# Kernel optimization log

Measured on AMD Instinct MI355X. Metric: run time of the kernel, lower is better.

The kernel has to match this reference:

```python
import jax, jax.numpy as jnp
import numpy as np

N_HEADS = 16
LN_EPS = 1e-6


def _mha(q_in, kv_in, mask, wq, bq, wk, bk, wv, bv, wo, bo):
    B, Sq, D = q_in.shape
    H = N_HEADS
    dh = D // H
    def split(x):  # [B,S,D] -> [B,H,S,dh]
        return x.reshape(B, -1, H, dh).transpose(0, 2, 1, 3)
    q = split(q_in @ wq + bq)
    k = split(kv_in @ wk + bk)
    v = split(kv_in @ wv + bv)
    scores = jnp.einsum('bhqd,bhkd->bhqk', q, k) / jnp.sqrt(jnp.asarray(dh, q.dtype))
    scores = scores + mask * (-1e9)
    attn = jax.nn.softmax(scores, axis=-1)
    out = jnp.einsum('bhqk,bhkd->bhqd', attn, v)
    out = out.transpose(0, 2, 1, 3).reshape(B, Sq, D)
    return out @ wo + bo


def _layer_norm(x, gamma, beta):
    mu = jnp.mean(x, axis=-1, keepdims=True)
    var = jnp.mean(jnp.square(x - mu), axis=-1, keepdims=True)
    return (x - mu) * jax.lax.rsqrt(var + LN_EPS) * gamma + beta


def setup_inputs() -> dict:
    key = jax.random.key(0)
    B, S_dec, S_enc, D, F = 4, 1024, 1024, 1024, 4096
    ks = jax.random.split(key, 16)
    s = 0.02
    inp = {
        'inputs': jax.random.normal(ks[0], (B, S_dec, D), jnp.float32),
        'enc_outputs': jax.random.normal(ks[1], (B, S_enc, D), jnp.float32),
        # causal look-ahead mask: 1 above diagonal -> -1e9 added to scores
        'mask_1': jnp.triu(jnp.ones((S_dec, S_dec), jnp.float32), k=1)[None, None],
        'mask_2': jnp.zeros((B, 1, 1, S_enc), jnp.float32),
    }
    names = ['wq1', 'wk1', 'wv1', 'wo1', 'wq2', 'wk2', 'wv2', 'wo2']
    for i, n in enumerate(names):
        inp[n] = jax.random.normal(ks[2 + i], (D, D), jnp.float32) * s
        inp['b' + n[1:]] = jnp.zeros((D,), jnp.float32)
    inp['w_ff1'] = jax.random.normal(ks[10], (D, F), jnp.float32) * s
    inp['b_ff1'] = jnp.zeros((F,), jnp.float32)
    inp['w_ff2'] = jax.random.normal(ks[11], (F, D), jnp.float32) * s
    inp['b_ff2'] = jnp.zeros((D,), jnp.float32)
    for i in (1, 2, 3):
        inp[f'g{i}'] = jnp.ones((D,), jnp.float32)
        inp[f'beta{i}'] = jnp.zeros((D,), jnp.float32)
    return inp


def reference(inputs, enc_outputs, mask_1, mask_2,
              wq1, bq1, wk1, bk1, wv1, bv1, wo1, bo1,
              wq2, bq2, wk2, bk2, wv2, bv2, wo2, bo2,
              w_ff1, b_ff1, w_ff2, b_ff2,
              g1, beta1, g2, beta2, g3, beta3):
    # causal self-attention + residual + LN (dropout inactive at inference)
    attn = _mha(inputs, inputs, mask_1, wq1, bq1, wk1, bk1, wv1, bv1, wo1, bo1)
    attn = _layer_norm(attn + inputs, g1, beta1)
    # encoder-decoder cross-attention + residual + LN
    attn2 = _mha(attn, enc_outputs, mask_2, wq2, bq2, wk2, bk2, wv2, bv2, wo2, bo2)
    attn2 = _layer_norm(attn2 + attn, g2, beta2)
    # FFN + residual + LN
    h = jax.nn.relu(attn2 @ w_ff1 + b_ff1)
    h = h @ w_ff2 + b_ff2
    return _layer_norm(h + attn2, g3, beta3)
```

## Files before the change

kernel.cpp:

```cpp
#include <hip/hip_runtime.h>
#include <stdint.h>

typedef unsigned short ushort_t;
typedef __attribute__((ext_vector_type(8))) short bf16x8;
typedef __attribute__((ext_vector_type(4))) float f32x4;
typedef __attribute__((ext_vector_type(4))) unsigned short us4;

#define DEV __device__ __forceinline__

DEV unsigned short f2bf(float f) {
  union { float f; unsigned u; } x; x.f = f;
  unsigned r = x.u + 0x7fffu + ((x.u >> 16) & 1u);
  return (unsigned short)(r >> 16);
}

DEV void gload16(const void* g, void* l) {
  __builtin_amdgcn_global_load_lds(
      (const __attribute__((address_space(1))) unsigned int*)g,
      (__attribute__((address_space(3))) unsigned int*)l, 16, 0, 0);
}

#define MFMA16 __builtin_amdgcn_mfma_f32_16x16x32_bf16

__global__ __launch_bounds__(256) void cast_bf16_kernel(
    const float* __restrict__ x, ushort_t* __restrict__ y, int n4) {
  int i = blockIdx.x * 256 + threadIdx.x;
  if (i >= n4) return;
  float4 v = ((const float4*)x)[i];
  us4 o; o.x = f2bf(v.x); o.y = f2bf(v.y); o.z = f2bf(v.z); o.w = f2bf(v.w);
  ((us4*)y)[i] = o;
}

__global__ __launch_bounds__(256) void reduce_cast_kernel(
    const float* __restrict__ p0, const float* __restrict__ p1,
    ushort_t* __restrict__ y, int n4) {
  int i = blockIdx.x * 256 + threadIdx.x;
  if (i >= n4) return;
  float4 a = ((const float4*)p0)[i];
  float4 b = ((const float4*)p1)[i];
  us4 o; o.x = f2bf(a.x + b.x); o.y = f2bf(a.y + b.y);
  o.z = f2bf(a.z + b.z); o.w = f2bf(a.w + b.w);
  ((us4*)y)[i] = o;
}

__global__ __launch_bounds__(256) void transpose_cast_kernel(
    const float* __restrict__ W, ushort_t* __restrict__ dst, int K, int N) {
  __shared__ float tile[64][65];
  int n0 = blockIdx.x * 64, k0 = blockIdx.y * 64;
  int tid = threadIdx.x;
#pragma unroll
  for (int it = 0; it < 16; ++it) {
    int idx = it * 256 + tid; int r = idx >> 6, c = idx & 63;
    tile[r][c] = W[(size_t)(k0 + r) * N + n0 + c];
  }
  __syncthreads();
#pragma unroll
  for (int it = 0; it < 16; ++it) {
    int idx = it * 256 + tid; int r = idx >> 6, c = idx & 63;
    dst[(size_t)(n0 + r) * K + k0 + c] = f2bf(tile[c][r]);
  }
}

struct Src8 { const float* p[8]; };
__global__ __launch_bounds__(256) void transpose_cast8_kernel(
    Src8 s, ushort_t* __restrict__ dst) {
  __shared__ float tile[64][65];
  const float* W = s.p[blockIdx.z];
  ushort_t* out = dst + (size_t)blockIdx.z * 1048576;
  int n0 = blockIdx.x * 64, k0 = blockIdx.y * 64;
  int tid = threadIdx.x;
#pragma unroll
  for (int it = 0; it < 16; ++it) {
    int idx = it * 256 + tid; int r = idx >> 6, c = idx & 63;
    tile[r][c] = W[(size_t)(k0 + r) * 1024 + n0 + c];
  }
  __syncthreads();
#pragma unroll
  for (int it = 0; it < 16; ++it) {
    int idx = it * 256 + tid; int r = idx >> 6, c = idx & 63;
    out[(size_t)(n0 + r) * 1024 + k0 + c] = f2bf(tile[c][r]);
  }
}

__global__ __launch_bounds__(256) void transpose_v_kernel(
    const ushort_t* __restrict__ V, int ldv, ushort_t* __restrict__ vT) {
  __shared__ ushort_t tile[64][65];
  int s0 = blockIdx.x * 64;
  int bh = blockIdx.y;
  int b = bh >> 4, h = bh & 15;
  int tid = threadIdx.x;
#pragma unroll
  for (int it = 0; it < 4; ++it) {
    int idx = it * 256 + tid; int r = idx >> 4, c = (idx & 15) * 4;
    us4 v = *(const us4*)&V[(size_t)(b * 1024 + s0 + r) * ldv + h * 64 + c];
    tile[r][c] = v.x; tile[r][c + 1] = v.y; tile[r][c + 2] = v.z; tile[r][c + 3] = v.w;
  }
  __syncthreads();
#pragma unroll
  for (int it = 0; it < 4; ++it) {
    int idx = it * 256 + tid; int r = idx >> 4, c = (idx & 15) * 4;
    us4 o; o.x = tile[c][r]; o.y = tile[c + 1][r]; o.z = tile[c + 2][r]; o.w = tile[c + 3][r];
    *(us4*)&vT[((size_t)bh * 64 + r) * 1024 + s0 + c] = o;
  }
}

template <int WF32, int WB16, int RELU>
__global__ __launch_bounds__(256, 2) void gemm_bt(
    const ushort_t* __restrict__ A, const ushort_t* __restrict__ Bt,
    const float* __restrict__ b0, const float* __restrict__ b1,
    const float* __restrict__ b2, const float* __restrict__ b3,
    float* __restrict__ Cf, ushort_t* __restrict__ Cb,
    int M, int N, int K, int Ks, long long pstr) {
  __shared__ ushort_t sA[4096];
  __shared__ ushort_t sB[4096];
  const int tid = threadIdx.x;
  const int w = tid >> 6, lane = tid & 63;
  const int lrow = lane & 15, lk = lane >> 4;
  const int m0 = blockIdx.x * 128, n0 = blockIdx.y * 128;
  const int kz = blockIdx.z * Ks;
  const int wr = w >> 1, wc = w & 1;
  f32x4 acc[4][4] = {};
  const int brow0 = (w * 1024 + lane * 16) >> 6;
  const int kbyte = (lane * 16) & 63;

  for (int kt = kz; kt < kz + Ks; kt += 32) {
    __syncthreads();
    const ushort_t* ga = A + (size_t)(m0 + brow0) * K + kt + (kbyte >> 1);
    gload16(ga, (char*)sA + w * 1024);
    gload16(ga + (size_t)64 * K, (char*)sA + 4096 + w * 1024);
    const ushort_t* gb = Bt + (size_t)(n0 + brow0) * K + kt + (kbyte >> 1);
    gload16(gb, (char*)sB + w * 1024);
    gload16(gb + (size_t)64 * K, (char*)sB + 4096 + w * 1024);
    __syncthreads();
    bf16x8 aF[4], bF[4];
#pragma unroll
    for (int t = 0; t < 4; ++t) {
      aF[t] = *(const bf16x8*)((const char*)sA + ((wr * 64 + t * 16 + lrow) << 6) + (lk << 4));
      bF[t] = *(const bf16x8*)((const char*)sB + ((wc * 64 + t * 16 + lrow) << 6) + (lk << 4));
    }
#pragma unroll
    for (int mt = 0; mt < 4; ++mt)
#pragma unroll
      for (int nt = 0; nt < 4; ++nt)
        acc[mt][nt] = MFMA16(aF[mt], bF[nt], acc[mt][nt], 0, 0, 0);
  }
  float* Cfz = Cf + (long long)blockIdx.z * pstr;
#pragma unroll
  for (int nt = 0; nt < 4; ++nt) {
    int col = n0 + wc * 64 + nt * 16 + lrow;
    int seg = col >> 10;
    const float* bp = seg == 0 ? b0 : seg == 1 ? b1 : seg == 2 ? b2 : b3;
    float bv = bp[col & 1023];
    if (blockIdx.z != 0) bv = 0.f;
#pragma unroll
    for (int mt = 0; mt < 4; ++mt) {
      int rowb = m0 + wr * 64 + mt * 16 + lk * 4;
#pragma unroll
      for (int j = 0; j < 4; ++j) {
        float v = acc[mt][nt][j] + bv;
        if (RELU) v = fmaxf(v, 0.f);
        size_t idx = (size_t)(rowb + j) * N + col;
        if (WF32) Cfz[idx] = v;
        if (WB16) Cb[idx] = f2bf(v);
      }
    }
  }
}

template <int WF32, int WB16, int RELU>
__global__ __launch_bounds__(512, 1) void gemm256(
    const ushort_t* __restrict__ A, const ushort_t* __restrict__ Bt,
    const float* __restrict__ b0, const float* __restrict__ b1,
    const float* __restrict__ b2, const float* __restrict__ b3,
    float* __restrict__ Cf, ushort_t* __restrict__ Cb,
    int M, int N, int K, int Ks, long long pstr) {
  extern __shared__ char L[];
  const int tid = threadIdx.x;
  const int w = tid >> 6, lane = tid & 63;
  const int lrow = lane & 15, lk = lane >> 4;
  const int wm = w >> 2, wn = w & 3;
  const int m0 = blockIdx.x * 256, n0 = blockIdx.y * 256;
  const int kz = blockIdx.z * Ks;
  const int nt = Ks >> 6;

  const int srow = w * 8 + (lane >> 3);
  const int gsw = (lane & 7) ^ ((lane >> 3) & 7);
  const ushort_t* srcA = A + (size_t)(m0 + srow) * K + kz + gsw * 8;
  const ushort_t* srcB = Bt + (size_t)(n0 + srow) * K + kz + gsw * 8;
  const int dstw = w * 1024;

#define STG(M_, T_)                                                   \
  do {                                                                \
    const ushort_t* g0 = ((M_) ? srcB : srcA) + (size_t)(T_) * 64;    \
    char* d_ = L + (((T_) & 1) << 16) + ((M_) << 15) + dstw;          \
    gload16(g0, d_);                                                  \
    gload16(g0 + (size_t)64 * K, d_ + 8192);                          \
    gload16(g0 + (size_t)128 * K, d_ + 16384);                        \
    gload16(g0 + (size_t)192 * K, d_ + 24576);                        \
  } while (0)

  f32x4 acc[8][4] = {};
  const int swz = (lrow & 7) << 4;
  const int k0b = (lk << 4) ^ swz;
  const int k1b = (64 + (lk << 4)) ^ swz;
  const int aBase = (wm * 128 + lrow) << 7;
  const int bBase = ((wn * 64 + lrow) << 7) + 32768;

  STG(0, 0); STG(1, 0); STG(0, 1);
  asm volatile("s_waitcnt vmcnt(4)" ::: "memory");
  __builtin_amdgcn_s_barrier();

  for (int t = 0; t < nt; ++t) {
    const int buf = (t & 1) << 16;
    const char* base = L + buf;
    bf16x8 aF[8], bF0, bF1;
    {
#pragma unroll
      for (int m = 0; m < 8; ++m) aF[m] = *(const bf16x8*)(base + aBase + m * 2048 + k0b);
      bF0 = *(const bf16x8*)(base + bBase + k0b);
      bF1 = *(const bf16x8*)(base + bBase + 2048 + k0b);
      if (t + 1 < nt) STG(1, t + 1);
      __builtin_amdgcn_s_barrier();
      __builtin_amdgcn_s_setprio(1);
#pragma unroll
      for (int m = 0; m < 8; ++m) {
        acc[m][0] = MFMA16(aF[m], bF0, acc[m][0], 0, 0, 0);
        acc[m][1] = MFMA16(aF[m], bF1, acc[m][1], 0, 0, 0);
      }
      __builtin_amdgcn_s_setprio(0);
      __builtin_amdgcn_s_barrier();
    }
    {
      bF0 = *(const bf16x8*)(base + bBase + 4096 + k0b);
      bF1 = *(const bf16x8*)(base + bBase + 6144 + k0b);
      __builtin_amdgcn_s_barrier();
      __builtin_amdgcn_s_setprio(1);
#pragma unroll
      for (int m = 0; m < 8; ++m) {
        acc[m][2] = MFMA16(aF[m], bF0, acc[m][2], 0, 0, 0);
        acc[m][3] = MFMA16(aF[m], bF1, acc[m][3], 0, 0, 0);
      }
      __builtin_amdgcn_s_setprio(0);
      __builtin_amdgcn_s_barrier();
    }
    {
#pragma unroll
      for (int m = 0; m < 8; ++m) aF[m] = *(const bf16x8*)(base + aBase + m * 2048 + k1b);
      bF0 = *(const bf16x8*)(base + bBase + k1b);
      bF1 = *(const bf16x8*)(base + bBase + 2048 + k1b);
      __builtin_amdgcn_s_barrier();
      __builtin_amdgcn_s_setprio(1);
#pragma unroll
      for (int m = 0; m < 8; ++m) {
        acc[m][0] = MFMA16(aF[m], bF0, acc[m][0], 0, 0, 0);
        acc[m][1] = MFMA16(aF[m], bF1, acc[m][1], 0, 0, 0);
      }
      __builtin_amdgcn_s_setprio(0);
      __builtin_amdgcn_s_barrier();
    }
    {
      bF0 = *(const bf16x8*)(base + bBase + 4096 + k1b);
      bF1 = *(const bf16x8*)(base + bBase + 6144 + k1b);
      if (t + 2 < nt) {
        STG(0, t + 2);
        asm volatile("s_waitcnt vmcnt(4)" ::: "memory");
      } else {
        asm volatile("s_waitcnt vmcnt(0)" ::: "memory");
      }
      __builtin_amdgcn_s_barrier();
      __builtin_amdgcn_s_setprio(1);
#pragma unroll
      for (int m = 0; m < 8; ++m) {
        acc[m][2] = MFMA16(aF[m], bF0, acc[m][2], 0, 0, 0);
        acc[m][3] = MFMA16(aF[m], bF1, acc[m][3], 0, 0, 0);
      }
      __builtin_amdgcn_s_setprio(0);
      __builtin_amdgcn_s_barrier();
    }
  }
#undef STG

  float* Cfz = Cf + (long long)blockIdx.z * pstr;
#pragma unroll
  for (int n = 0; n < 4; ++n) {
    int col = n0 + wn * 64 + n * 16 + lrow;
    int seg = col >> 10;
    const float* bp = seg == 0 ? b0 : seg == 1 ? b1 : seg == 2 ? b2 : b3;
    float bv = bp[col & 1023];
    if (blockIdx.z != 0) bv = 0.f;
#pragma unroll
    for (int m = 0; m < 8; ++m) {
      int rowb = m0 + wm * 128 + m * 16 + lk * 4;
#pragma unroll
      for (int j = 0; j < 4; ++j) {
        float v = acc[m][n][j] + bv;
        if (RELU) v = fmaxf(v, 0.f);
        size_t idx = (size_t)(rowb + j) * N + col;
        if (WF32) Cfz[idx] = v;
        if (WB16) Cb[idx] = f2bf(v);
      }
    }
  }
}

template <int CAUSAL>
__global__ __launch_bounds__(256, 4) void attn_kernel(
    const ushort_t* __restrict__ Q, int ldq,
    const ushort_t* __restrict__ Kp, int ldk,
    const ushort_t* __restrict__ vT,
    const float* __restrict__ mask2,
    ushort_t* __restrict__ O) {
  __shared__ ushort_t sK[2][4096];
  __shared__ ushort_t sV[2][4096];
  __shared__ ushort_t sP[4][1024];
  const int bh = blockIdx.x, qb = blockIdx.y;
  const int b = bh >> 4, h = bh & 15;
  const int tid = threadIdx.x, w = tid >> 6, lane = tid & 63;
  const int lrow = lane & 15, lk = lane >> 4;

  const ushort_t* qptr = Q + (size_t)(b * 1024 + qb * 64 + w * 16 + lrow) * ldq + h * 64 + lk * 8;
  bf16x8 qF0 = *(const bf16x8*)qptr;
  bf16x8 qF1 = *(const bf16x8*)(qptr + 32);
  f32x4 oacc[4] = {};
  float m_ = -3.0e38f, l_ = 0.f;
  const int nkb = CAUSAL ? (qb + 1) : 16;
  const float C = 0.18033688011112042f;

  const int sr = w * 16 + (lane >> 3);
  const int scb = (((lane & 7) ^ (lane >> 3)) * 16);
  const ushort_t* kbase = Kp + (size_t)(b * 1024 + sr) * ldk + h * 64 + (scb >> 1);
  const ushort_t* vbase = vT + ((size_t)bh * 64 + sr) * 1024 + (scb >> 1);
  char* dstK0 = (char*)sK[0] + w * 2048;
  char* dstV0 = (char*)sV[0] + w * 2048;

#define STAGE(kb_, bufi)                                              \
  do {                                                                \
    const ushort_t* gk = kbase + (size_t)(kb_) * 64 * ldk;            \
    gload16(gk, dstK0 + (bufi) * 8192);                               \
    gload16(gk + (size_t)8 * ldk, dstK0 + (bufi) * 8192 + 1024);      \
    const ushort_t* gv = vbase + (kb_) * 64;                          \
    gload16(gv, dstV0 + (bufi) * 8192);                               \
    gload16(gv + (size_t)8 * 1024, dstV0 + (bufi) * 8192 + 1024);     \
  } while (0)

  STAGE(0, 0);
  const int swz = (lrow & 7) << 4;

  for (int kb = 0; kb < nkb; ++kb) {
    const int buf = kb & 1;
    __syncthreads();
    if (kb + 1 < nkb) STAGE(kb + 1, buf ^ 1);

    const char* kB = (const char*)sK[buf];
    const char* vB = (const char*)sV[buf];
    f32x4 sc[4];
    __builtin_amdgcn_s_setprio(1);
#pragma unroll
    for (int kt = 0; kt < 4; ++kt) {
      const char* rp = kB + ((kt * 16 + lrow) << 7);
      bf16x8 k0 = *(const bf16x8*)(rp + ((lk * 16) ^ swz));
      bf16x8 k1 = *(const bf16x8*)(rp + ((64 + lk * 16) ^ swz));
      f32x4 z = {};
      z = MFMA16(k0, qF0, z, 0, 0, 0);
      sc[kt] = MFMA16(k1, qF1, z, 0, 0, 0);
    }
    __builtin_amdgcn_s_setprio(0);
    if (CAUSAL) {
      if (kb == qb) {
        int ql = w * 16 + lrow;
#pragma unroll
        for (int kt = 0; kt < 4; ++kt)
#pragma unroll
          for (int j = 0; j < 4; ++j)
            if (kt * 16 + lk * 4 + j > ql) sc[kt][j] = -3.0e38f;
      }
    } else {
#pragma unroll
      for (int kt = 0; kt < 4; ++kt) {
        float4 mv = *(const float4*)&mask2[b * 1024 + kb * 64 + kt * 16 + lk * 4];
        sc[kt][0] = fmaf(mv.x, -8e9f, sc[kt][0]);
        sc[kt][1] = fmaf(mv.y, -8e9f, sc[kt][1]);
        sc[kt][2] = fmaf(mv.z, -8e9f, sc[kt][2]);
        sc[kt][3] = fmaf(mv.w, -8e9f, sc[kt][3]);
      }
    }
    float pmax = fmaxf(fmaxf(fmaxf(sc[0][0], sc[0][1]), fmaxf(sc[0][2], sc[0][3])),
                       fmaxf(fmaxf(sc[1][0], sc[1][1]), fmaxf(sc[1][2], sc[1][3])));
    pmax = fmaxf(pmax, fmaxf(fmaxf(fmaxf(sc[2][0], sc[2][1]), fmaxf(sc[2][2], sc[2][3])),
                             fmaxf(fmaxf(sc[3][0], sc[3][1]), fmaxf(sc[3][2], sc[3][3]))));
    pmax = fmaxf(pmax, __shfl_xor(pmax, 16));
    pmax = fmaxf(pmax, __shfl_xor(pmax, 32));
    if (__any(pmax - m_ > 64.f)) {
      float mnew = fmaxf(m_, pmax);
      float scale = __builtin_exp2f((m_ - mnew) * C);
      l_ *= scale;
      m_ = mnew;
#pragma unroll
      for (int j = 0; j < 4; ++j) {
        float sj = __shfl(scale, lk * 4 + j);
        oacc[0][j] *= sj; oacc[1][j] *= sj; oacc[2][j] *= sj; oacc[3][j] *= sj;
      }
    }
    const float mC = m_ * C;
    float ps = 0.f;
#pragma unroll
    for (int kt = 0; kt < 4; ++kt)
#pragma unroll
      for (int j = 0; j < 4; ++j) {
        float e = __builtin_exp2f(fmaf(sc[kt][j], C, -mC));
        sc[kt][j] = e;
        ps += e;
      }
    ps += __shfl_xor(ps, 16);
    ps += __shfl_xor(ps, 32);
    l_ += ps;
    char* bp = (char*)sP[w] + lrow * 128;
#pragma unroll
    for (int kt = 0; kt < 4; ++kt) {
      unsigned d0, d1;
      asm("v_cvt_pk_bf16_f32 %0, %1, %2" : "=v"(d0) : "v"(sc[kt][0]), "v"(sc[kt][1]));
      asm("v_cvt_pk_bf16_f32 %0, %1, %2" : "=v"(d1) : "v"(sc[kt][2]), "v"(sc[kt][3]));
      uint2 dd; dd.x = d0; dd.y = d1;
      *(uint2*)(bp + ((kt * 32 + lk * 8) ^ swz)) = dd;
    }
    bf16x8 pF0 = *(const bf16x8*)(bp + ((lk * 16) ^ swz));
    bf16x8 pF1 = *(const bf16x8*)(bp + ((64 + lk * 16) ^ swz));
    __builtin_amdgcn_s_setprio(1);
#pragma unroll
    for (int t = 0; t < 4; ++t) {
      const char* rp = vB + ((t * 16 + lrow) << 7);
      bf16x8 v0 = *(const bf16x8*)(rp + ((lk * 16) ^ swz));
      bf16x8 v1 = *(const bf16x8*)(rp + ((64 + lk * 16) ^ swz));
      oacc[t] = MFMA16(pF0, v0, oacc[t], 0, 0, 0);
      oacc[t] = MFMA16(pF1, v1, oacc[t], 0, 0, 0);
    }
    __builtin_amdgcn_s_setprio(0);
  }
#undef STAGE
#pragma unroll
  for (int j = 0; j < 4; ++j) {
    float lj = __shfl(l_, lk * 4 + j);
    float invl = 1.f / lj;
    int row = qb * 64 + w * 16 + lk * 4 + j;
    ushort_t* op = O + (size_t)(b * 1024 + row) * 1024 + h * 64;
#pragma unroll
    for (int t = 0; t < 4; ++t) op[t * 16 + lrow] = f2bf(oacc[t][j] * invl);
  }
}

template <int WB16, int NPART>
__global__ __launch_bounds__(256) void ln_kernel(
    const float* __restrict__ p0, const float* __restrict__ p1,
    const float* __restrict__ p2, const float* __restrict__ p3,
    const float* __restrict__ r,
    const float* __restrict__ g, const float* __restrict__ be,
    float* __restrict__ yf, ushort_t* __restrict__ yb) {
  int row = blockIdx.x, tid = threadIdx.x;
  size_t off = (size_t)row * 1024;
  float4 va = ((const float4*)(p0 + off))[tid];
  if (NPART >= 2) {
    float4 t = ((const float4*)(p1 + off))[tid];
    va.x += t.x; va.y += t.y; va.z += t.z; va.w += t.w;
  }
  if (NPART >= 4) {
    float4 t2 = ((const float4*)(p2 + off))[tid];
    float4 t3 = ((const float4*)(p3 + off))[tid];
    va.x += t2.x + t3.x; va.y += t2.y + t3.y;
    va.z += t2.z + t3.z; va.w += t2.w + t3.w;
  }
  float4 vb = ((const float4*)(r + off))[tid];
  float x0 = va.x + vb.x, x1 = va.y + vb.y, x2 = va.z + vb.z, x3 = va.w + vb.w;
  float s = x0 + x1 + x2 + x3;
  float s2 = x0 * x0 + x1 * x1 + x2 * x2 + x3 * x3;
#pragma unroll
  for (int o = 1; o < 64; o <<= 1) { s += __shfl_xor(s, o); s2 += __shfl_xor(s2, o); }
  __shared__ float sh[8];
  if ((tid & 63) == 0) { sh[tid >> 6] = s; sh[4 + (tid >> 6)] = s2; }
  __syncthreads();
  s = sh[0] + sh[1] + sh[2] + sh[3];
  s2 = sh[4] + sh[5] + sh[6] + sh[7];
  float mu = s * 0.0009765625f;
  float var = s2 * 0.0009765625f - mu * mu;
  float inv = rsqrtf(var + 1e-6f);
  float4 gv = ((const float4*)g)[tid];
  float4 bv = ((const float4*)be)[tid];
  float y0 = (x0 - mu) * inv * gv.x + bv.x;
  float y1 = (x1 - mu) * inv * gv.y + bv.y;
  float y2 = (x2 - mu) * inv * gv.z + bv.z;
  float y3 = (x3 - mu) * inv * gv.w + bv.w;
  ((float4*)(yf + off))[tid] = make_float4(y0, y1, y2, y3);
  if (WB16) {
    us4 o; o.x = f2bf(y0); o.y = f2bf(y1); o.z = f2bf(y2); o.w = f2bf(y3);
    ((us4*)(yb + off))[tid] = o;
  }
}

extern "C" void kernel_launch(void* const* d_in, const int* in_sizes, int n_in,
                              void* d_out, int out_size, void* d_ws, size_t ws_size,
                              hipStream_t stream) {
  (void)in_sizes; (void)n_in; (void)out_size; (void)ws_size;
  const float* inputs = (const float*)d_in[0];
  const float* enc    = (const float*)d_in[1];
  const float* mask2  = (const float*)d_in[3];
  const float* wq1 = (const float*)d_in[4];  const float* bq1 = (const float*)d_in[5];
  const float* wk1 = (const float*)d_in[6];  const float* bk1 = (const float*)d_in[7];
  const float* wv1 = (const float*)d_in[8];  const float* bv1 = (const float*)d_in[9];
  const float* wo1 = (const float*)d_in[10]; const float* bo1 = (const float*)d_in[11];
  const float* wq2 = (const float*)d_in[12]; const float* bq2 = (const float*)d_in[13];
  const float* wk2 = (const float*)d_in[14]; const float* bk2 = (const float*)d_in[15];
  const float* wv2 = (const float*)d_in[16]; const float* bv2 = (const float*)d_in[17];
  const float* wo2 = (const float*)d_in[18]; const float* bo2 = (const float*)d_in[19];
  const float* wff1 = (const float*)d_in[20]; const float* bff1 = (const float*)d_in[21];
  const float* wff2 = (const float*)d_in[22]; const float* bff2 = (const float*)d_in[23];
  const float* g1 = (const float*)d_in[24]; const float* be1 = (const float*)d_in[25];
  const float* g2 = (const float*)d_in[26]; const float* be2 = (const float*)d_in[27];
  const float* g3 = (const float*)d_in[28]; const float* be3 = (const float*)d_in[29];

  char* ws = (char*)d_ws;
  const size_t MB = 1024 * 1024;
  const size_t W1M = 1048576;
  ushort_t* wt    = (ushort_t*)ws;
  ushort_t* xb    = (ushort_t*)(ws + 32 * MB);
  ushort_t* encb  = (ushort_t*)(ws + 40 * MB);
  ushort_t* qkvb  = (ushort_t*)(ws + 48 * MB);
  ushort_t* vtb   = (ushort_t*)(ws + 72 * MB);
  ushort_t* attnb = (ushort_t*)(ws + 80 * MB);
  ushort_t* y1b   = (ushort_t*)(ws + 88 * MB);
  ushort_t* y2b   = (ushort_t*)(ws + 96 * MB);
  float*    c1f   = (float*)(ws + 104 * MB);
  float*    p48f  = (float*)(ws + 48 * MB);
  float*    y1f   = (float*)(ws + 120 * MB);
  float*    y2f   = (float*)(ws + 136 * MB);
  ushort_t* q2b   = (ushort_t*)(ws + 32 * MB);
  ushort_t* kv2b  = (ushort_t*)(ws + 56 * MB);
  ushort_t* hb    = (ushort_t*)(ws + 32 * MB);
  float*    pff   = (float*)(ws + 72 * MB);
  float* outf = (float*)d_out;
  const long long PELEMS = 4 * 1024 * 1024;
  const long long P48OFF = (long long)(p48f - c1f);

  cast_bf16_kernel<<<4096, 256, 0, stream>>>(inputs, xb, 1048576);
  cast_bf16_kernel<<<4096, 256, 0, stream>>>(enc, encb, 1048576);
  Src8 s8; s8.p[0] = wq1; s8.p[1] = wk1; s8.p[2] = wv1; s8.p[3] = wo1;
           s8.p[4] = wq2; s8.p[5] = wk2; s8.p[6] = wv2; s8.p[7] = wo2;
  transpose_cast8_kernel<<<dim3(16, 16, 8), 256, 0, stream>>>(s8, wt);
  transpose_cast_kernel<<<dim3(64, 16), 256, 0, stream>>>(wff1, wt + 8 * W1M, 1024, 4096);
  transpose_cast_kernel<<<dim3(16, 64), 256, 0, stream>>>(wff2, wt + 12 * W1M, 4096, 1024);

  gemm256<0, 1, 0><<<dim3(16, 12, 1), 512, 131072, stream>>>(
      xb, wt, bq1, bk1, bv1, bv1, nullptr, qkvb, 4096, 3072, 1024, 1024, 0);
  transpose_v_kernel<<<dim3(16, 64), 256, 0, stream>>>(qkvb + 2048, 3072, vtb);
  attn_kernel<1><<<dim3(64, 16), 256, 0, stream>>>(
      qkvb, 3072, qkvb + 1024, 3072, vtb, nullptr, attnb);
  gemm_bt<1, 0, 0><<<dim3(32, 8, 2), 256, 0, stream>>>(
      attnb, wt + 3 * W1M, bo1, bo1, bo1, bo1, c1f, nullptr, 4096, 1024, 1024, 512, P48OFF);
  ln_kernel<1, 2><<<4096, 256, 0, stream>>>(c1f, p48f, nullptr, nullptr,
                                            inputs, g1, be1, y1f, y1b);

  gemm_bt<1, 0, 0><<<dim3(32, 8, 2), 256, 0, stream>>>(
      y1b, wt + 4 * W1M, bq2, bq2, bq2, bq2, c1f, nullptr, 4096, 1024, 1024, 512, P48OFF);
  reduce_cast_kernel<<<4096, 256, 0, stream>>>(c1f, p48f, q2b, 1048576);
  gemm_bt<0, 1, 0><<<dim3(32, 16, 1), 256, 0, stream>>>(
      encb, wt + 5 * W1M, bk2, bv2, bk2, bk2, nullptr, kv2b, 4096, 2048, 1024, 1024, 0);
  transpose_v_kernel<<<dim3(16, 64), 256, 0, stream>>>(kv2b + 1024, 2048, vtb);
  attn_kernel<0><<<dim3(64, 16), 256, 0, stream>>>(
      q2b, 1024, kv2b, 2048, vtb, mask2, attnb);
  gemm_bt<1, 0, 0><<<dim3(32, 8, 2), 256, 0, stream>>>(
      attnb, wt + 7 * W1M, bo2, bo2, bo2, bo2, c1f, nullptr, 4096, 1024, 1024, 512, P48OFF);
  ln_kernel<1, 2><<<4096, 256, 0, stream>>>(c1f, p48f, nullptr, nullptr,
                                            y1f, g2, be2, y2f, y2b);

  gemm256<0, 1, 1><<<dim3(16, 16, 1), 512, 131072, stream>>>(
      y2b, wt + 8 * W1M, bff1, bff1 + 1024, bff1 + 2048, bff1 + 3072,
      nullptr, hb, 4096, 4096, 1024, 1024, 0);
  gemm256<1, 0, 0><<<dim3(16, 4, 4), 512, 131072, stream>>>(
      hb, wt + 12 * W1M, bff2, bff2, bff2, bff2, pff, nullptr,
      4096, 1024, 4096, 1024, PELEMS);
  ln_kernel<0, 4><<<4096, 256, 0, stream>>>(pff, pff + PELEMS, pff + 2 * PELEMS,
                                            pff + 3 * PELEMS, y2f, g3, be3, outf, nullptr);
}
```

Baseline: 363.6 us.

## Process 128 query rows per attention block to reuse K/V tiles

Each attention block now covers 128 query rows instead of 64, with every wave owning two 16-row groups that share the same staged K and V tiles in LDS. This halves the grid and the global K/V traffic per query, at the cost of more registers, a lower occupancy hint (3 instead of 4) and a doubled P scratch buffer. Under the causal mask, groups that lie entirely above the diagonal skip their softmax and PV MFMAs. The QK MFMAs still run for every group. Fewer blocks may load-balance worse, especially for the causal kernel where work per block varies.

```diff
diff --git a/kernel.cpp b/kernel.cpp
--- a/kernel.cpp
+++ b/kernel.cpp
@@ -304,7 +304,7 @@
 }
 
 template <int CAUSAL>
-__global__ __launch_bounds__(256, 4) void attn_kernel(
+__global__ __launch_bounds__(256, 3) void attn_kernel(
     const ushort_t* __restrict__ Q, int ldq,
     const ushort_t* __restrict__ Kp, int ldk,
     const ushort_t* __restrict__ vT,
@@ -312,18 +312,24 @@
     ushort_t* __restrict__ O) {
   __shared__ ushort_t sK[2][4096];
   __shared__ ushort_t sV[2][4096];
-  __shared__ ushort_t sP[4][1024];
+  __shared__ ushort_t sP[4][2048];
   const int bh = blockIdx.x, qb = blockIdx.y;
   const int b = bh >> 4, h = bh & 15;
   const int tid = threadIdx.x, w = tid >> 6, lane = tid & 63;
   const int lrow = lane & 15, lk = lane >> 4;
-
-  const ushort_t* qptr = Q + (size_t)(b * 1024 + qb * 64 + w * 16 + lrow) * ldq + h * 64 + lk * 8;
-  bf16x8 qF0 = *(const bf16x8*)qptr;
-  bf16x8 qF1 = *(const bf16x8*)(qptr + 32);
-  f32x4 oacc[4] = {};
-  float m_ = -3.0e38f, l_ = 0.f;
-  const int nkb = CAUSAL ? (qb + 1) : 16;
+  const int q0 = qb * 128 + w * 32;
+
+  bf16x8 qF[2][2];
+#pragma unroll
+  for (int g = 0; g < 2; ++g) {
+    const ushort_t* qptr =
+        Q + (size_t)(b * 1024 + q0 + g * 16 + lrow) * ldq + h * 64 + lk * 8;
+    qF[g][0] = *(const bf16x8*)qptr;
+    qF[g][1] = *(const bf16x8*)(qptr + 32);
+  }
+  f32x4 oacc[2][4] = {};
+  float m_[2] = {-3.0e38f, -3.0e38f}, l_[2] = {0.f, 0.f};
+  const int nkb = CAUSAL ? (qb * 2 + 2) : 16;
   const float C = 0.18033688011112042f;
 
   const int sr = w * 16 + (lane >> 3);
@@ -353,99 +359,135 @@
 
     const char* kB = (const char*)sK[buf];
     const char* vB = (const char*)sV[buf];
-    f32x4 sc[4];
+    bool skip[2], edge[2];
+#pragma unroll
+    for (int g = 0; g < 2; ++g) {
+      int qming = q0 + g * 16;
+      skip[g] = CAUSAL && (kb * 64 > qming + 15);
+      edge[g] = CAUSAL && !skip[g] && (kb * 64 + 63 > qming);
+    }
+    f32x4 sc[2][4];
     __builtin_amdgcn_s_setprio(1);
 #pragma unroll
     for (int kt = 0; kt < 4; ++kt) {
       const char* rp = kB + ((kt * 16 + lrow) << 7);
       bf16x8 k0 = *(const bf16x8*)(rp + ((lk * 16) ^ swz));
       bf16x8 k1 = *(const bf16x8*)(rp + ((64 + lk * 16) ^ swz));
-      f32x4 z = {};
-      z = MFMA16(k0, qF0, z, 0, 0, 0);
-      sc[kt] = MFMA16(k1, qF1, z, 0, 0, 0);
+      f32x4 z0 = {};
+      z0 = MFMA16(k0, qF[0][0], z0, 0, 0, 0);
+      sc[0][kt] = MFMA16(k1, qF[0][1], z0, 0, 0, 0);
+      f32x4 z1 = {};
+      z1 = MFMA16(k0, qF[1][0], z1, 0, 0, 0);
+      sc[1][kt] = MFMA16(k1, qF[1][1], z1, 0, 0, 0);
     }
     __builtin_amdgcn_s_setprio(0);
-    if (CAUSAL) {
-      if (kb == qb) {
-        int ql = w * 16 + lrow;
-#pragma unroll
-        for (int kt = 0; kt < 4; ++kt)
-#pragma unroll
-          for (int j = 0; j < 4; ++j)
-            if (kt * 16 + lk * 4 + j > ql) sc[kt][j] = -3.0e38f;
-      }
-    } else {
+    float4 mv[4];
+    if (!CAUSAL) {
+#pragma unroll
+      for (int kt = 0; kt < 4; ++kt)
+        mv[kt] = *(const float4*)&mask2[b * 1024 + kb * 64 + kt * 16 + lk * 4];
+    }
+#pragma unroll
+    for (int g = 0; g < 2; ++g) {
+      if (skip[g]) continue;
+      if (CAUSAL) {
+        if (edge[g]) {
+          int qrel = q0 + g * 16 + lrow - kb * 64;
+#pragma unroll
+          for (int kt = 0; kt < 4; ++kt)
+#pragma unroll
+            for (int j = 0; j < 4; ++j)
+              if (kt * 16 + lk * 4 + j > qrel) sc[g][kt][j] = -3.0e38f;
+        }
+      } else {
+#pragma unroll
+        for (int kt = 0; kt < 4; ++kt) {
+          sc[g][kt][0] = fmaf(mv[kt].x, -8e9f, sc[g][kt][0]);
+          sc[g][kt][1] = fmaf(mv[kt].y, -8e9f, sc[g][kt][1]);
+          sc[g][kt][2] = fmaf(mv[kt].z, -8e9f, sc[g][kt][2]);
+          sc[g][kt][3] = fmaf(mv[kt].w, -8e9f, sc[g][kt][3]);
+        }
+      }
+      float pmax = fmaxf(
+          fmaxf(fmaxf(sc[g][0][0], sc[g][0][1]), fmaxf(sc[g][0][2], sc[g][0][3])),
+          fmaxf(fmaxf(sc[g][1][0], sc[g][1][1]), fmaxf(sc[g][1][2], sc[g][1][3])));
+      pmax = fmaxf(pmax, fmaxf(
+          fmaxf(fmaxf(sc[g][2][0], sc[g][2][1]), fmaxf(sc[g][2][2], sc[g][2][3])),
+          fmaxf(fmaxf(sc[g][3][0], sc[g][3][1]), fmaxf(sc[g][3][2], sc[g][3][3]))));
+      pmax = fmaxf(pmax, __shfl_xor(pmax, 16));
+      pmax = fmaxf(pmax, __shfl_xor(pmax, 32));
+      if (__any(pmax - m_[g] > 64.f)) {
+        float mnew = fmaxf(m_[g], pmax);
+        float scale = __builtin_exp2f((m_[g] - mnew) * C);
+        l_[g] *= scale;
+        m_[g] = mnew;
+#pragma unroll
+        for (int j = 0; j < 4; ++j) {
+          float sj = __shfl(scale, lk * 4 + j);
+          oacc[g][0][j] *= sj; oacc[g][1][j] *= sj;
+          oacc[g][2][j] *= sj; oacc[g][3][j] *= sj;
+        }
+      }
+      const float mC = m_[g] * C;
+      float ps = 0.f;
+#pragma unroll
+      for (int kt = 0; kt < 4; ++kt)
+#pragma unroll
+        for (int j = 0; j < 4; ++j) {
+          float e = __builtin_exp2f(fmaf(sc[g][kt][j], C, -mC));
+          sc[g][kt][j] = e;
+          ps += e;
+        }
+      ps += __shfl_xor(ps, 16);
+      ps += __shfl_xor(ps, 32);
+      l_[g] += ps;
+      char* bp = (char*)sP[w] + (g * 16 + lrow) * 128;
 #pragma unroll
       for (int kt = 0; kt < 4; ++kt) {
-        float4 mv = *(const float4*)&mask2[b * 1024 + kb * 64 + kt * 16 + lk * 4];
-        sc[kt][0] = fmaf(mv.x, -8e9f, sc[kt][0]);
-        sc[kt][1] = fmaf(mv.y, -8e9f, sc[kt][1]);
-        sc[kt][2] = fmaf(mv.z, -8e9f, sc[kt][2]);
-        sc[kt][3] = fmaf(mv.w, -8e9f, sc[kt][3]);
-      }
-    }
-    float pmax = fmaxf(fmaxf(fmaxf(sc[0][0], sc[0][1]), fmaxf(sc[0][2], sc[0][3])),
-                       fmaxf(fmaxf(sc[1][0], sc[1][1]), fmaxf(sc[1][2], sc[1][3])));
-    pmax = fmaxf(pmax, fmaxf(fmaxf(fmaxf(sc[2][0], sc[2][1]), fmaxf(sc[2][2], sc[2][3])),
-                             fmaxf(fmaxf(sc[3][0], sc[3][1]), fmaxf(sc[3][2], sc[3][3]))));
-    pmax = fmaxf(pmax, __shfl_xor(pmax, 16));
-    pmax = fmaxf(pmax, __shfl_xor(pmax, 32));
-    if (__any(pmax - m_ > 64.f)) {
-      float mnew = fmaxf(m_, pmax);
-      float scale = __builtin_exp2f((m_ - mnew) * C);
-      l_ *= scale;
-      m_ = mnew;
-#pragma unroll
-      for (int j = 0; j < 4; ++j) {
-        float sj = __shfl(scale, lk * 4 + j);
-        oacc[0][j] *= sj; oacc[1][j] *= sj; oacc[2][j] *= sj; oacc[3][j] *= sj;
-      }
-    }
-    const float mC = m_ * C;
-    float ps = 0.f;
-#pragma unroll
-    for (int kt = 0; kt < 4; ++kt)
-#pragma unroll
-      for (int j = 0; j < 4; ++j) {
-        float e = __builtin_exp2f(fmaf(sc[kt][j], C, -mC));
-        sc[kt][j] = e;
-        ps += e;
-      }
-    ps += __shfl_xor(ps, 16);
-    ps += __shfl_xor(ps, 32);
-    l_ += ps;
-    char* bp = (char*)sP[w] + lrow * 128;
-#pragma unroll
-    for (int kt = 0; kt < 4; ++kt) {
-      unsigned d0, d1;
-      asm("v_cvt_pk_bf16_f32 %0, %1, %2" : "=v"(d0) : "v"(sc[kt][0]), "v"(sc[kt][1]));
-      asm("v_cvt_pk_bf16_f32 %0, %1, %2" : "=v"(d1) : "v"(sc[kt][2]), "v"(sc[kt][3]));
-      uint2 dd; dd.x = d0; dd.y = d1;
-      *(uint2*)(bp + ((kt * 32 + lk * 8) ^ swz)) = dd;
-    }
-    bf16x8 pF0 = *(const bf16x8*)(bp + ((lk * 16) ^ swz));
-    bf16x8 pF1 = *(const bf16x8*)(bp + ((64 + lk * 16) ^ swz));
+        unsigned d0, d1;
+        asm("v_cvt_pk_bf16_f32 %0, %1, %2" : "=v"(d0) : "v"(sc[g][kt][0]), "v"(sc[g][kt][1]));
+        asm("v_cvt_pk_bf16_f32 %0, %1, %2" : "=v"(d1) : "v"(sc[g][kt][2]), "v"(sc[g][kt][3]));
+        uint2 dd; dd.x = d0; dd.y = d1;
+        *(uint2*)(bp + ((kt * 32 + lk * 8) ^ swz)) = dd;
+      }
+    }
+    bf16x8 pF[2][2];
+#pragma unroll
+    for (int g = 0; g < 2; ++g) {
+      if (skip[g]) continue;
+      const char* pB = (const char*)sP[w] + (g * 16 + lrow) * 128;
+      pF[g][0] = *(const bf16x8*)(pB + ((lk * 16) ^ swz));
+      pF[g][1] = *(const bf16x8*)(pB + ((64 + lk * 16) ^ swz));
+    }
     __builtin_amdgcn_s_setprio(1);
 #pragma unroll
     for (int t = 0; t < 4; ++t) {
       const char* rp = vB + ((t * 16 + lrow) << 7);
       bf16x8 v0 = *(const bf16x8*)(rp + ((lk * 16) ^ swz));
       bf16x8 v1 = *(const bf16x8*)(rp + ((64 + lk * 16) ^ swz));
-      oacc[t] = MFMA16(pF0, v0, oacc[t], 0, 0, 0);
-      oacc[t] = MFMA16(pF1, v1, oacc[t], 0, 0, 0);
+      if (!skip[0]) {
+        oacc[0][t] = MFMA16(pF[0][0], v0, oacc[0][t], 0, 0, 0);
+        oacc[0][t] = MFMA16(pF[0][1], v1, oacc[0][t], 0, 0, 0);
+      }
+      if (!skip[1]) {
+        oacc[1][t] = MFMA16(pF[1][0], v0, oacc[1][t], 0, 0, 0);
+        oacc[1][t] = MFMA16(pF[1][1], v1, oacc[1][t], 0, 0, 0);
+      }
     }
     __builtin_amdgcn_s_setprio(0);
   }
 #undef STAGE
 #pragma unroll
-  for (int j = 0; j < 4; ++j) {
-    float lj = __shfl(l_, lk * 4 + j);
-    float invl = 1.f / lj;
-    int row = qb * 64 + w * 16 + lk * 4 + j;
-    ushort_t* op = O + (size_t)(b * 1024 + row) * 1024 + h * 64;
-#pragma unroll
-    for (int t = 0; t < 4; ++t) op[t * 16 + lrow] = f2bf(oacc[t][j] * invl);
-  }
+  for (int g = 0; g < 2; ++g)
+#pragma unroll
+    for (int j = 0; j < 4; ++j) {
+      float lj = __shfl(l_[g], lk * 4 + j);
+      float invl = 1.f / lj;
+      int row = q0 + g * 16 + lk * 4 + j;
+      ushort_t* op = O + (size_t)(b * 1024 + row) * 1024 + h * 64;
+#pragma unroll
+      for (int t = 0; t < 4; ++t) op[t * 16 + lrow] = f2bf(oacc[g][t][j] * invl);
+    }
 }
 
 template <int WB16, int NPART>
@@ -550,7 +592,7 @@
   gemm256<0, 1, 0><<<dim3(16, 12, 1), 512, 131072, stream>>>(
       xb, wt, bq1, bk1, bv1, bv1, nullptr, qkvb, 4096, 3072, 1024, 1024, 0);
   transpose_v_kernel<<<dim3(16, 64), 256, 0, stream>>>(qkvb + 2048, 3072, vtb);
-  attn_kernel<1><<<dim3(64, 16), 256, 0, stream>>>(
+  attn_kernel<1><<<dim3(64, 8), 256, 0, stream>>>(
       qkvb, 3072, qkvb + 1024, 3072, vtb, nullptr, attnb);
   gemm_bt<1, 0, 0><<<dim3(32, 8, 2), 256, 0, stream>>>(
       attnb, wt + 3 * W1M, bo1, bo1, bo1, bo1, c1f, nullptr, 4096, 1024, 1024, 512, P48OFF);
@@ -563,7 +605,7 @@
   gemm_bt<0, 1, 0><<<dim3(32, 16, 1), 256, 0, stream>>>(
       encb, wt + 5 * W1M, bk2, bv2, bk2, bk2, nullptr, kv2b, 4096, 2048, 1024, 1024, 0);
   transpose_v_kernel<<<dim3(16, 64), 256, 0, stream>>>(kv2b + 1024, 2048, vtb);
-  attn_kernel<0><<<dim3(64, 16), 256, 0, stream>>>(
+  attn_kernel<0><<<dim3(64, 8), 256, 0, stream>>>(
       q2b, 1024, kv2b, 2048, vtb, mask2, attnb);
   gemm_bt<1, 0, 0><<<dim3(32, 8, 2), 256, 0, stream>>>(
       attnb, wt + 7 * W1M, bo2, bo2, bo2, bo2, c1f, nullptr, 4096, 1024, 1024, 512, P48OFF);
```

Result: slower. 372.4 us (+2.4%).
